# Kernel tuning notes

Hardware: AMD Instinct MI355X
Metric: run time of the kernel (lower is better)

## Reference

```python
import jax, jax.numpy as jnp
import numpy as np

B, S, HID = 2, 2048, 2048
H, HKV, D = 16, 4, 128        # num_heads, num_kv_heads, head_dim
G = H // HKV                   # GQA group size
CLIP = 8.0                     # clip_qkv
THETA = 10000.0                # rope_theta_within_seq
N_SEQS = 8                     # max_num_sequences


def setup_inputs() -> dict:
    key = jax.random.key(0)
    ks = jax.random.split(key, 6)
    hidden_states = jax.random.normal(ks[0], (B, S, HID), dtype=jnp.float32)
    within_seq_position_ids = jnp.broadcast_to(jnp.arange(S, dtype=jnp.int64), (B, S))
    global_position_ids = jnp.broadcast_to(jnp.arange(S, dtype=jnp.int64), (B, S))
    sequence_ids = jnp.sort(jax.random.randint(ks[1], (B, S), 0, N_SEQS, dtype=jnp.int64), axis=-1)
    scale = 0.02
    Wq = jax.random.normal(ks[2], (H * D, HID), dtype=jnp.float32) * scale
    Wk = jax.random.normal(ks[3], (HKV * D, HID), dtype=jnp.float32) * scale
    Wv = jax.random.normal(ks[4], (HKV * D, HID), dtype=jnp.float32) * scale
    Wo = jax.random.normal(ks[5], (HID, H * D), dtype=jnp.float32) * scale
    return {"hidden_states": hidden_states,
            "within_seq_position_ids": within_seq_position_ids,
            "global_position_ids": global_position_ids,
            "sequence_ids": sequence_ids,
            "Wq": Wq, "Wk": Wk, "Wv": Wv, "Wo": Wo}


def _rotate_half(x):
    x1, x2 = jnp.split(x, 2, axis=-1)
    return jnp.concatenate((-x2, x1), axis=-1)


def _rope_cos_sin(position_ids, dtype):
    # inv_freq: [D/2]
    inv_freq = THETA ** (-(jnp.arange(0, D, 2, dtype=jnp.float32) / D))
    angles = position_ids.astype(jnp.float32)[..., None] * inv_freq  # [B,S,D/2]
    angles = jnp.concatenate((angles, angles), axis=-1)              # [B,S,D]
    # unsqueeze head dim -> [B,S,1,D]
    return jnp.cos(angles)[:, :, None, :].astype(dtype), jnp.sin(angles)[:, :, None, :].astype(dtype)


def reference(hidden_states, within_seq_position_ids, global_position_ids, sequence_ids, Wq, Wk, Wv, Wo):
    b, s, _ = hidden_states.shape
    q = (hidden_states @ Wq.T).reshape(b, s, H, D)
    k = (hidden_states @ Wk.T).reshape(b, s, HKV, D)
    v = (hidden_states @ Wv.T).reshape(b, s, HKV, D)
    # clip_qkv
    q = jnp.clip(q, -CLIP, CLIP)
    k = jnp.clip(k, -CLIP, CLIP)
    v = jnp.clip(v, -CLIP, CLIP)
    # RoPE (within_seq layer -> within_seq_position_ids)
    cos, sin = _rope_cos_sin(within_seq_position_ids, q.dtype)
    q = q * cos + _rotate_half(q) * sin
    k = k * cos + _rotate_half(k) * sin
    # GQA: group queries by kv head instead of materializing repeat_kv
    q = q.transpose(0, 2, 1, 3).reshape(b, HKV, G, s, D)  # [B,HKV,G,S,D]
    k = k.transpose(0, 2, 1, 3)                            # [B,HKV,S,D]
    v = v.transpose(0, 2, 1, 3)
    scores = jnp.einsum('bhgqd,bhkd->bhgqk', q, k) / jnp.sqrt(jnp.asarray(D, q.dtype))
    # block-diagonal (same sequence) causal mask
    qi = jnp.arange(s)
    causal = qi[:, None] >= qi[None, :]                    # [S,S]
    same_seq = sequence_ids[:, :, None] == sequence_ids[:, None, :]  # [B,S,S]
    mask = (causal[None] & same_seq)[:, None, None, :, :]  # [B,1,1,S,S]
    scores = jnp.where(mask, scores, jnp.finfo(scores.dtype).min)
    attn = jax.nn.softmax(scores, axis=-1)
    out = jnp.einsum('bhgqk,bhkd->bhgqd', attn, v)         # [B,HKV,G,S,D]
    out = out.reshape(b, H, s, D).transpose(0, 2, 1, 3).reshape(b, s, H * D)
    return out @ Wo.T
```

## Files before the change

kernel.cpp:

```cpp
#include <hip/hip_runtime.h>
#include <hip/hip_bf16.h>

typedef __hip_bfloat16 bf16;
typedef __attribute__((ext_vector_type(8))) short bf16x8;
typedef __attribute__((ext_vector_type(4))) float f32x4;

#define MFMA_BF16(a, b, c) __builtin_amdgcn_mfma_f32_16x16x32_bf16((a), (b), (c), 0, 0, 0)

#define B_   2
#define S_   2048
#define HID_ 2048
#define H_   16
#define HKV_ 4
#define D_   128

#define GLOAD_LDS(gptr, lptr) \
  __builtin_amdgcn_global_load_lds((const __attribute__((address_space(1))) void*)(gptr), \
                                   (__attribute__((address_space(3))) void*)(lptr), 16, 0, 0)

template <int N>
__device__ __forceinline__ void vmw() {
  if constexpr (N == 0)      asm volatile("s_waitcnt vmcnt(0)" ::: "memory");
  else if constexpr (N == 4) asm volatile("s_waitcnt vmcnt(4)" ::: "memory");
  else if constexpr (N == 5) asm volatile("s_waitcnt vmcnt(5)" ::: "memory");
  else                       asm volatile("s_waitcnt vmcnt(6)" ::: "memory");
}

__device__ __forceinline__ void blk_barrier() {
  __builtin_amdgcn_sched_barrier(0);
  __builtin_amdgcn_s_barrier();
  __builtin_amdgcn_sched_barrier(0);
}

__global__ void cvt_all(const float* __restrict__ hidden, const float* __restrict__ Wq,
                        const float* __restrict__ Wk, const float* __restrict__ Wv,
                        const float* __restrict__ Wo, const int* __restrict__ seq,
                        bf16* __restrict__ Xb, bf16* __restrict__ Wqkv, bf16* __restrict__ Wob,
                        int* __restrict__ sstart) {
  if (blockIdx.x >= 18432) {
    int t = (blockIdx.x - 18432) * 256 + threadIdx.x;
    int b = t >> 11, s = t & (S_ - 1);
    const int* sb = seq + b * S_;
    int sid = sb[s];
    int lo = 0, hi = s;
    while (lo < hi) {
      int mid = (lo + hi) >> 1;
      if (sb[mid] < sid) lo = mid + 1; else hi = mid;
    }
    sstart[t] = lo;
    return;
  }
  long long i4 = (long long)blockIdx.x * 256 + threadIdx.x;
  const float* src; bf16* dst; long long off;
  if (i4 < 2097152)      { src = hidden; dst = Xb;             off = i4; }
  else if (i4 < 3145728) { src = Wq;     dst = Wqkv;           off = i4 - 2097152; }
  else if (i4 < 3407872) { src = Wk;     dst = Wqkv + 4194304; off = i4 - 3145728; }
  else if (i4 < 3670016) { src = Wv;     dst = Wqkv + 5242880; off = i4 - 3407872; }
  else                   { src = Wo;     dst = Wob;            off = i4 - 3670016; }
  float4 v = *reinterpret_cast<const float4*>(src + off * 4);
  alignas(8) bf16 t[4];
  t[0] = __float2bfloat16(v.x);
  t[1] = __float2bfloat16(v.y);
  t[2] = __float2bfloat16(v.z);
  t[3] = __float2bfloat16(v.w);
  *reinterpret_cast<short4*>(dst + off * 4) = *reinterpret_cast<const short4*>(t);
}

template <int BM, int BN, int OUT_BF16>
__global__ __launch_bounds__(512, 2) void gemm8p(const bf16* __restrict__ A,
                                                 const bf16* __restrict__ Bw,
                                                 void* __restrict__ Cout,
                                                 int M, int N, int K) {
  constexpr int MR = BM / 32;
  constexpr int NR = BN / 64;
  constexpr int LA = BM / 128;
  constexpr int QD = NR + 2;

  __shared__ bf16 As[2][2][BM * 32];
  __shared__ bf16 Bs[2][BN * 64];

  const int tid  = threadIdx.x;
  const int lane = tid & 63;
  const int w    = tid >> 6;
  const int wr   = w >> 2;
  const int wc   = w & 3;
  const int ln15 = lane & 15, g = lane >> 4;

  const int nwg = gridDim.x;
  int bid = blockIdx.x;
  bid = (bid & 7) * (nwg >> 3) + (bid >> 3);
  const int nbn = N / BN;
  const int m0 = (bid / nbn) * BM;
  const int n0 = (bid % nbn) * BN;

  f32x4 acc[MR][NR] = {};

  auto stageA = [&](int db, int kh, int t) {
    int kc = t * 64 + kh * 32;
#pragma unroll
    for (int r = 0; r < LA; r++) {
      int sIdx = r * 512 + tid;
      int row = sIdx >> 2;
      int ss = (sIdx & 3) ^ ((row >> 1) & 3);
      GLOAD_LDS(A + (size_t)(m0 + row) * K + kc + ss * 8, &As[db][kh][(r * 512 + w * 64) * 8]);
    }
  };
  auto stageB = [&](int db, int t) {
#pragma unroll
    for (int r = 0; r < NR; r++) {
      int sIdx = r * 512 + tid;
      int row = sIdx >> 3;
      int cs = (sIdx & 7) ^ (row & 7);
      GLOAD_LDS(Bw + (size_t)(n0 + row) * K + t * 64 + cs * 8, &Bs[db][(size_t)(r * 512 + w * 64) * 8]);
    }
  };

  bf16x8 af[4], bfr[NR];
  auto rdA = [&](int db, int kh, int mb) {
#pragma unroll
    for (int m = 0; m < 4; m++) {
      int row = wr * (BM / 2) + (mb + m) * 16 + ln15;
      af[m] = *reinterpret_cast<const bf16x8*>(&As[db][kh][row * 32 + ((g ^ ((row >> 1) & 3)) << 3)]);
    }
  };
  auto rdB = [&](int db, int kh) {
#pragma unroll
    for (int n = 0; n < NR; n++) {
      int row = wc * (BN / 4) + n * 16 + ln15;
      int sl = ((kh << 2) + g) ^ (row & 7);
      bfr[n] = *reinterpret_cast<const bf16x8*>(&Bs[db][row * 64 + sl * 8]);
    }
  };
  auto MF = [&](int mb) {
    __builtin_amdgcn_s_setprio(1);
#pragma unroll
    for (int m = 0; m < 4; m++)
#pragma unroll
      for (int n = 0; n < NR; n++)
        acc[mb + m][n] = MFMA_BF16(af[m], bfr[n], acc[mb + m][n]);
    __builtin_amdgcn_s_setprio(0);
  };

  const int NT = K >> 6;

  stageA(0, 0, 0);
  stageA(0, 1, 0);
  stageB(0, 0);
  stageA(1, 0, 1);
  stageB(1, 1);
  vmw<QD>();
  blk_barrier();

  for (int T = 0; T < NT; ++T) {
    const int db = T & 1, dn = db ^ 1;

    rdA(db, 0, 0); rdB(db, 0);
    if (T + 1 < NT) stageA(dn, 1, T + 1);
    MF(0); blk_barrier();

    rdA(db, 0, 4);
    MF(4); blk_barrier();

    rdA(db, 1, 0); rdB(db, 1);
    if (T + 2 < NT) stageA(db, 0, T + 2);
    MF(0); blk_barrier();

    rdA(db, 1, 4);
    if (T + 2 < NT) stageB(db, T + 2);
    MF(4);
    if (T + 1 < NT) {
      if (T == NT - 2) vmw<0>(); else vmw<QD>();
    }
    blk_barrier();
  }

#pragma unroll
  for (int m = 0; m < MR; m++)
#pragma unroll
    for (int n = 0; n < NR; n++)
#pragma unroll
      for (int r = 0; r < 4; r++) {
        int row = m0 + wr * (BM / 2) + m * 16 + g * 4 + r;
        int col = n0 + wc * (BN / 4) + n * 16 + ln15;
        if constexpr (OUT_BF16) {
          ((bf16*)Cout)[(size_t)row * N + col] = __float2bfloat16(acc[m][n][r]);
        } else {
          ((float*)Cout)[(size_t)row * N + col] = acc[m][n][r];
        }
      }
}

__global__ __launch_bounds__(256) void qkv_post(const bf16* __restrict__ QKV,
                                                const int* __restrict__ wpos,
                                                bf16* __restrict__ Qs,
                                                bf16* __restrict__ Ks) {
  const int row = blockIdx.x;
  const int b = row >> 11, s = row & (S_ - 1);
  const int t = threadIdx.x;
  const bf16* R = QKV + (size_t)row * 3072;
  const float pos = (float)wpos[row];
  const float kln = 0.14391156831212787f;
  const float qscale = 0.08838834764831845f;

  const int i = t & 63;
  const int hq = t >> 6;
  float sn, cs;
  {
    float ang = pos * expf(-(float)i * kln);
    sincosf(ang, &sn, &cs);
  }

#pragma unroll
  for (int it = 0; it < 4; it++) {
    int h = hq + it * 4;
    float x1 = __bfloat162float(R[h * 128 + i]);
    float x2 = __bfloat162float(R[h * 128 + 64 + i]);
    x1 = fminf(fmaxf(x1, -8.f), 8.f);
    x2 = fminf(fmaxf(x2, -8.f), 8.f);
    float y1 = (x1 * cs - x2 * sn) * qscale;
    float y2 = (x2 * cs + x1 * sn) * qscale;
    size_t qb = ((size_t)(b * H_ + h) * S_ + s) * D_;
    Qs[qb + i]      = __float2bfloat16(y1);
    Qs[qb + 64 + i] = __float2bfloat16(y2);
  }
  {
    int kh = hq;
    float x1 = __bfloat162float(R[2048 + kh * 128 + i]);
    float x2 = __bfloat162float(R[2048 + kh * 128 + 64 + i]);
    x1 = fminf(fmaxf(x1, -8.f), 8.f);
    x2 = fminf(fmaxf(x2, -8.f), 8.f);
    float y1 = x1 * cs - x2 * sn;
    float y2 = x2 * cs + x1 * sn;
    size_t kb = ((size_t)(b * HKV_ + kh) * S_ + s) * D_;
    Ks[kb + i]      = __float2bfloat16(y1);
    Ks[kb + 64 + i] = __float2bfloat16(y2);
  }
}

__global__ __launch_bounds__(256) void vt_trans(const bf16* __restrict__ QKV,
                                                bf16* __restrict__ Vt) {
  __shared__ bf16 Tl[64][132];
  const int t = threadIdx.x;
  const int blk = blockIdx.x;
  const int st = blk & 31, kvh = (blk >> 5) & 3, b = blk >> 7;
  const int s0 = st * 64;

#pragma unroll
  for (int p = 0; p < 8; p++) {
    int r = p * 8 + (t >> 5);
    int c = (t & 31) * 4;
    short4 v = *reinterpret_cast<const short4*>(QKV + (size_t)(b * S_ + s0 + r) * 3072 + 2560 + kvh * 128 + c);
    alignas(8) bf16 e[4];
    *reinterpret_cast<short4*>(e) = v;
#pragma unroll
    for (int k = 0; k < 4; k++) {
      float x = __bfloat162float(e[k]);
      x = fminf(fmaxf(x, -8.f), 8.f);
      Tl[r][c + k] = __float2bfloat16(x);
    }
  }
  __syncthreads();

  if (t < 128) {
    const int d = t;
    bf16* dst = Vt + ((size_t)(b * HKV_ + kvh) * D_ + d) * S_ + s0;
#pragma unroll
    for (int j = 0; j < 64; j += 8) {
      alignas(16) bf16 v[8];
#pragma unroll
      for (int k = 0; k < 8; k++) v[k] = Tl[j + k][d];
      *reinterpret_cast<short4*>(dst + j)     = *reinterpret_cast<const short4*>(&v[0]);
      *reinterpret_cast<short4*>(dst + j + 4) = *reinterpret_cast<const short4*>(&v[4]);
    }
  }
}

__global__ __launch_bounds__(256) void attn_fwd(const bf16* __restrict__ Qs,
                                                const bf16* __restrict__ Ks,
                                                const bf16* __restrict__ Vt,
                                                const int* __restrict__ sstart,
                                                bf16* __restrict__ att) {
  __shared__ bf16 Kl[2][32 * 128];
  __shared__ bf16 Vl[2][128 * 32];
  __shared__ bf16 Plds[4][2][16 * 32];

  const int tid = threadIdx.x;
  const int lane = tid & 63, w = tid >> 6;
  const int ln15 = lane & 15, g = lane >> 4;

  const int wg = ((blockIdx.x & 7) << 6) | (blockIdx.x >> 3);
  const int qt  = wg & 63;
  const int kvh = (wg >> 6) & 3;
  const int b   = wg >> 8;
  const int h   = kvh * 4 + w;
  const int q0  = qt * 32;
  const int qa  = q0 + ln15;
  const int qb  = q0 + 16 + ln15;

  const bf16* Qbase = Qs + (size_t)(b * H_ + h) * S_ * D_;
  bf16x8 qfa[4], qfb[4];
#pragma unroll
  for (int c = 0; c < 4; c++) {
    qfa[c] = *reinterpret_cast<const bf16x8*>(Qbase + (size_t)qa * D_ + c * 32 + g * 8);
    qfb[c] = *reinterpret_cast<const bf16x8*>(Qbase + (size_t)qb * D_ + c * 32 + g * 8);
  }

  const int sQa = sstart[b * S_ + qa];
  const int sQb = sstart[b * S_ + qb];
  const int kstart = __builtin_amdgcn_readfirstlane(__shfl(sQa, 0));
  const int kend = q0 + 31;

  const bf16* Kb = Ks + (size_t)(b * HKV_ + kvh) * S_ * D_;
  const bf16* Vb = Vt + (size_t)(b * HKV_ + kvh) * D_ * S_;

  auto stage = [&](int buf, int kb) {
#pragma unroll
    for (int p = 0; p < 2; p++) {
      int slot = p * 256 + tid;
      int row = slot >> 4;
      int cs = (slot & 15) ^ (row & 15);
      int gr = min(kb + row, S_ - 1);
      GLOAD_LDS(Kb + (size_t)gr * D_ + cs * 8, &Kl[buf][(p * 256 + w * 64) * 8]);
    }
#pragma unroll
    for (int p = 0; p < 2; p++) {
      int slot = p * 256 + tid;
      int d = slot >> 2, c = slot & 3;
      int cs = c ^ (d & 3);
      int gcol = min(kb + cs * 8, S_ - 8);
      GLOAD_LDS(Vb + (size_t)d * S_ + gcol, &Vl[buf][(p * 256 + w * 64) * 8]);
    }
  };

  float ma = -1e30f, la = 0.f, mb = -1e30f, lb = 0.f;
  f32x4 oa[8] = {}, ob[8] = {};

  auto softmax = [&](const f32x4& s0, const f32x4& s1, int qi, int sQ, int kb,
                     float& m, float& lsum, f32x4 (&o)[8], bf16* pdst) {
    float sc[8];
    float tmax = -1e30f;
#pragma unroll
    for (int r = 0; r < 4; r++) {
      int k0i = kb + g * 4 + r;
      int k1i = k0i + 16;
      float x0 = (k0i >= sQ && k0i <= qi) ? s0[r] : -1e30f;
      float x1 = (k1i >= sQ && k1i <= qi) ? s1[r] : -1e30f;
      sc[r] = x0;
      sc[4 + r] = x1;
      tmax = fmaxf(tmax, fmaxf(x0, x1));
    }
    tmax = fmaxf(tmax, __shfl_xor(tmax, 16));
    tmax = fmaxf(tmax, __shfl_xor(tmax, 32));
    float mn  = fmaxf(m, tmax);
    float fac = __expf(m - mn);
    float ps = 0.f;
    alignas(16) bf16 pb[8];
#pragma unroll
    for (int i2 = 0; i2 < 8; i2++) {
      float p = (sc[i2] < -1e29f) ? 0.f : __expf(sc[i2] - mn);
      ps += p;
      pb[i2] = __float2bfloat16(p);
    }
    ps += __shfl_xor(ps, 16);
    ps += __shfl_xor(ps, 32);
    lsum = lsum * fac + ps;
    m = mn;
#pragma unroll
    for (int t2 = 0; t2 < 8; t2++) o[t2] *= fac;
    *reinterpret_cast<short4*>(pdst + ln15 * 32 + g * 4)      = *reinterpret_cast<const short4*>(&pb[0]);
    *reinterpret_cast<short4*>(pdst + ln15 * 32 + 16 + g * 4) = *reinterpret_cast<const short4*>(&pb[4]);
  };

  stage(0, kstart);
  int buf = 0;
  for (int kb = kstart; kb <= kend; kb += 32) {
    __syncthreads();
    if (kb + 32 <= kend) stage(buf ^ 1, kb + 32);

    bf16x8 kf0[4], kf1[4];
#pragma unroll
    for (int c = 0; c < 4; c++) {
      kf0[c] = *reinterpret_cast<const bf16x8*>(&Kl[buf][ln15 * 128 + (((c * 4 + g) ^ ln15) << 3)]);
      kf1[c] = *reinterpret_cast<const bf16x8*>(&Kl[buf][(16 + ln15) * 128 + (((c * 4 + g) ^ ln15) << 3)]);
    }
    f32x4 sa0 = {0.f, 0.f, 0.f, 0.f}, sa1 = sa0, sb0 = sa0, sb1 = sa0;
#pragma unroll
    for (int c = 0; c < 4; c++) {
      sa0 = MFMA_BF16(kf0[c], qfa[c], sa0);
      sa1 = MFMA_BF16(kf1[c], qfa[c], sa1);
      sb0 = MFMA_BF16(kf0[c], qfb[c], sb0);
      sb1 = MFMA_BF16(kf1[c], qfb[c], sb1);
    }

    softmax(sa0, sa1, qa, sQa, kb, ma, la, oa, &Plds[w][0][0]);
    softmax(sb0, sb1, qb, sQb, kb, mb, lb, ob, &Plds[w][1][0]);
    __builtin_amdgcn_wave_barrier();
    bf16x8 pfa = *reinterpret_cast<const bf16x8*>(&Plds[w][0][ln15 * 32 + g * 8]);
    bf16x8 pfb = *reinterpret_cast<const bf16x8*>(&Plds[w][1][ln15 * 32 + g * 8]);

#pragma unroll
    for (int t2 = 0; t2 < 8; t2++) {
      int d = t2 * 16 + ln15;
      bf16x8 vf = *reinterpret_cast<const bf16x8*>(&Vl[buf][d * 32 + ((g ^ (ln15 & 3)) << 3)]);
      oa[t2] = MFMA_BF16(vf, pfa, oa[t2]);
      ob[t2] = MFMA_BF16(vf, pfb, ob[t2]);
    }
    __builtin_amdgcn_wave_barrier();
    buf ^= 1;
  }

  float inva = 1.f / la;
  float invb = 1.f / lb;
#pragma unroll
  for (int t2 = 0; t2 < 8; t2++)
#pragma unroll
    for (int r = 0; r < 4; r++) {
      int d = t2 * 16 + g * 4 + r;
      att[((size_t)(b * S_ + qa)) * (H_ * D_) + h * D_ + d] = __float2bfloat16(oa[t2][r] * inva);
      att[((size_t)(b * S_ + qb)) * (H_ * D_) + h * D_ + d] = __float2bfloat16(ob[t2][r] * invb);
    }
}

extern "C" void kernel_launch(void* const* d_in, const int* in_sizes, int n_in,
                              void* d_out, int out_size, void* d_ws, size_t ws_size,
                              hipStream_t stream) {
  const float* hidden = (const float*)d_in[0];
  const int* wpos = (const int*)d_in[1];
  const int* seq = (const int*)d_in[3];
  const float* Wq = (const float*)d_in[4];
  const float* Wk = (const float*)d_in[5];
  const float* Wv = (const float*)d_in[6];
  const float* Wo = (const float*)d_in[7];

  char* ws = (char*)d_ws;
  bf16* Xb   = (bf16*)(ws);
  bf16* Wqkv = (bf16*)(ws + 16777216);
  bf16* Wob  = (bf16*)(ws + 29360128);
  bf16* QKVb = (bf16*)(ws + 37748736);
  bf16* Ksb  = (bf16*)(ws + 62914560);
  bf16* Vtb  = (bf16*)(ws + 67108864);
  int*  sst  = (int*)(ws + 71303168);
  bf16* Qsb  = Xb;
  bf16* attb = QKVb;

  cvt_all<<<dim3(18464), dim3(256), 0, stream>>>(hidden, Wq, Wk, Wv, Wo, seq, Xb, Wqkv, Wob, sst);

  gemm8p<256, 192, 1><<<dim3(256), dim3(512), 0, stream>>>(Xb, Wqkv, (void*)QKVb, 4096, 3072, 2048);

  qkv_post<<<dim3(4096), dim3(256), 0, stream>>>(QKVb, wpos, Qsb, Ksb);
  vt_trans<<<dim3(256), dim3(256), 0, stream>>>(QKVb, Vtb);

  attn_fwd<<<dim3(512), dim3(256), 0, stream>>>(Qsb, Ksb, Vtb, sst, attb);

  gemm8p<128, 256, 0><<<dim3(256), dim3(512), 0, stream>>>(attb, Wob, d_out, 4096, 2048, 2048);
}
```

Before: 164.5 us.

## Fuse V transpose into qkv_post and load K/V fragments directly from global

Folds the vt_trans kernel into qkv_post as extra blocks, removing one kernel launch. The attention kernel drops its double-buffered LDS staging of K and V tiles and the per-iteration block barrier. Each wave now reads its K and V MFMA fragments straight from global memory. This avoids LDS traffic and synchronisation, but the four waves in a block, which share a KV head, each fetch the same tiles redundantly. There is also no software prefetch, so global load latency may be exposed.

```diff
diff --git a/kernel.cpp b/kernel.cpp
--- a/kernel.cpp
+++ b/kernel.cpp
@@ -193,10 +193,47 @@
 __global__ __launch_bounds__(256) void qkv_post(const bf16* __restrict__ QKV,
                                                 const int* __restrict__ wpos,
                                                 bf16* __restrict__ Qs,
-                                                bf16* __restrict__ Ks) {
+                                                bf16* __restrict__ Ks,
+                                                bf16* __restrict__ Vt) {
+  __shared__ bf16 Tl[64][132];
+  const int t = threadIdx.x;
+
+  if (blockIdx.x >= 4096) {
+    const int blk = blockIdx.x - 4096;
+    const int st = blk & 31, kvh = (blk >> 5) & 3, b = blk >> 7;
+    const int s0 = st * 64;
+#pragma unroll
+    for (int p = 0; p < 8; p++) {
+      int r = p * 8 + (t >> 5);
+      int c = (t & 31) * 4;
+      short4 v = *reinterpret_cast<const short4*>(QKV + (size_t)(b * S_ + s0 + r) * 3072 + 2560 + kvh * 128 + c);
+      alignas(8) bf16 e[4];
+      *reinterpret_cast<short4*>(e) = v;
+#pragma unroll
+      for (int k = 0; k < 4; k++) {
+        float x = __bfloat162float(e[k]);
+        x = fminf(fmaxf(x, -8.f), 8.f);
+        Tl[r][c + k] = __float2bfloat16(x);
+      }
+    }
+    __syncthreads();
+    if (t < 128) {
+      const int d = t;
+      bf16* dst = Vt + ((size_t)(b * HKV_ + kvh) * D_ + d) * S_ + s0;
+#pragma unroll
+      for (int j = 0; j < 64; j += 8) {
+        alignas(16) bf16 v[8];
+#pragma unroll
+        for (int k = 0; k < 8; k++) v[k] = Tl[j + k][d];
+        *reinterpret_cast<short4*>(dst + j)     = *reinterpret_cast<const short4*>(&v[0]);
+        *reinterpret_cast<short4*>(dst + j + 4) = *reinterpret_cast<const short4*>(&v[4]);
+      }
+    }
+    return;
+  }
+
   const int row = blockIdx.x;
   const int b = row >> 11, s = row & (S_ - 1);
-  const int t = threadIdx.x;
   const bf16* R = QKV + (size_t)row * 3072;
   const float pos = (float)wpos[row];
   const float kln = 0.14391156831212787f;
@@ -237,51 +274,11 @@
   }
 }
 
-__global__ __launch_bounds__(256) void vt_trans(const bf16* __restrict__ QKV,
-                                                bf16* __restrict__ Vt) {
-  __shared__ bf16 Tl[64][132];
-  const int t = threadIdx.x;
-  const int blk = blockIdx.x;
-  const int st = blk & 31, kvh = (blk >> 5) & 3, b = blk >> 7;
-  const int s0 = st * 64;
-
-#pragma unroll
-  for (int p = 0; p < 8; p++) {
-    int r = p * 8 + (t >> 5);
-    int c = (t & 31) * 4;
-    short4 v = *reinterpret_cast<const short4*>(QKV + (size_t)(b * S_ + s0 + r) * 3072 + 2560 + kvh * 128 + c);
-    alignas(8) bf16 e[4];
-    *reinterpret_cast<short4*>(e) = v;
-#pragma unroll
-    for (int k = 0; k < 4; k++) {
-      float x = __bfloat162float(e[k]);
-      x = fminf(fmaxf(x, -8.f), 8.f);
-      Tl[r][c + k] = __float2bfloat16(x);
-    }
-  }
-  __syncthreads();
-
-  if (t < 128) {
-    const int d = t;
-    bf16* dst = Vt + ((size_t)(b * HKV_ + kvh) * D_ + d) * S_ + s0;
-#pragma unroll
-    for (int j = 0; j < 64; j += 8) {
-      alignas(16) bf16 v[8];
-#pragma unroll
-      for (int k = 0; k < 8; k++) v[k] = Tl[j + k][d];
-      *reinterpret_cast<short4*>(dst + j)     = *reinterpret_cast<const short4*>(&v[0]);
-      *reinterpret_cast<short4*>(dst + j + 4) = *reinterpret_cast<const short4*>(&v[4]);
-    }
-  }
-}
-
 __global__ __launch_bounds__(256) void attn_fwd(const bf16* __restrict__ Qs,
                                                 const bf16* __restrict__ Ks,
                                                 const bf16* __restrict__ Vt,
                                                 const int* __restrict__ sstart,
                                                 bf16* __restrict__ att) {
-  __shared__ bf16 Kl[2][32 * 128];
-  __shared__ bf16 Vl[2][128 * 32];
   __shared__ bf16 Plds[4][2][16 * 32];
 
   const int tid = threadIdx.x;
@@ -313,25 +310,6 @@
   const bf16* Kb = Ks + (size_t)(b * HKV_ + kvh) * S_ * D_;
   const bf16* Vb = Vt + (size_t)(b * HKV_ + kvh) * D_ * S_;
 
-  auto stage = [&](int buf, int kb) {
-#pragma unroll
-    for (int p = 0; p < 2; p++) {
-      int slot = p * 256 + tid;
-      int row = slot >> 4;
-      int cs = (slot & 15) ^ (row & 15);
-      int gr = min(kb + row, S_ - 1);
-      GLOAD_LDS(Kb + (size_t)gr * D_ + cs * 8, &Kl[buf][(p * 256 + w * 64) * 8]);
-    }
-#pragma unroll
-    for (int p = 0; p < 2; p++) {
-      int slot = p * 256 + tid;
-      int d = slot >> 2, c = slot & 3;
-      int cs = c ^ (d & 3);
-      int gcol = min(kb + cs * 8, S_ - 8);
-      GLOAD_LDS(Vb + (size_t)d * S_ + gcol, &Vl[buf][(p * 256 + w * 64) * 8]);
-    }
-  };
-
   float ma = -1e30f, la = 0.f, mb = -1e30f, lb = 0.f;
   f32x4 oa[8] = {}, ob[8] = {};
 
@@ -371,17 +349,19 @@
     *reinterpret_cast<short4*>(pdst + ln15 * 32 + 16 + g * 4) = *reinterpret_cast<const short4*>(&pb[4]);
   };
 
-  stage(0, kstart);
-  int buf = 0;
   for (int kb = kstart; kb <= kend; kb += 32) {
-    __syncthreads();
-    if (kb + 32 <= kend) stage(buf ^ 1, kb + 32);
-
+    bf16x8 vf[8];
+#pragma unroll
+    for (int t2 = 0; t2 < 8; t2++)
+      vf[t2] = *reinterpret_cast<const bf16x8*>(Vb + (size_t)(t2 * 16 + ln15) * S_ + kb + g * 8);
+
+    const bf16* Kr0 = Kb + (size_t)(kb + ln15) * D_;
+    const bf16* Kr1 = Kb + (size_t)(kb + 16 + ln15) * D_;
     bf16x8 kf0[4], kf1[4];
 #pragma unroll
     for (int c = 0; c < 4; c++) {
-      kf0[c] = *reinterpret_cast<const bf16x8*>(&Kl[buf][ln15 * 128 + (((c * 4 + g) ^ ln15) << 3)]);
-      kf1[c] = *reinterpret_cast<const bf16x8*>(&Kl[buf][(16 + ln15) * 128 + (((c * 4 + g) ^ ln15) << 3)]);
+      kf0[c] = *reinterpret_cast<const bf16x8*>(Kr0 + c * 32 + g * 8);
+      kf1[c] = *reinterpret_cast<const bf16x8*>(Kr1 + c * 32 + g * 8);
     }
     f32x4 sa0 = {0.f, 0.f, 0.f, 0.f}, sa1 = sa0, sb0 = sa0, sb1 = sa0;
 #pragma unroll
@@ -400,13 +380,10 @@
 
 #pragma unroll
     for (int t2 = 0; t2 < 8; t2++) {
-      int d = t2 * 16 + ln15;
-      bf16x8 vf = *reinterpret_cast<const bf16x8*>(&Vl[buf][d * 32 + ((g ^ (ln15 & 3)) << 3)]);
-      oa[t2] = MFMA_BF16(vf, pfa, oa[t2]);
-      ob[t2] = MFMA_BF16(vf, pfb, ob[t2]);
+      oa[t2] = MFMA_BF16(vf[t2], pfa, oa[t2]);
+      ob[t2] = MFMA_BF16(vf[t2], pfb, ob[t2]);
     }
     __builtin_amdgcn_wave_barrier();
-    buf ^= 1;
   }
 
   float inva = 1.f / la;
@@ -447,8 +424,7 @@
 
   gemm8p<256, 192, 1><<<dim3(256), dim3(512), 0, stream>>>(Xb, Wqkv, (void*)QKVb, 4096, 3072, 2048);
 
-  qkv_post<<<dim3(4096), dim3(256), 0, stream>>>(QKVb, wpos, Qsb, Ksb);
-  vt_trans<<<dim3(256), dim3(256), 0, stream>>>(QKVb, Vtb);
+  qkv_post<<<dim3(4352), dim3(256), 0, stream>>>(QKVb, wpos, Qsb, Ksb, Vtb);
 
   attn_fwd<<<dim3(512), dim3(256), 0, stream>>>(Qsb, Ksb, Vtb, sst, attb);
 
```

Result: slower. 221.1 us (+34.4%).
